# Kernel optimization log

Measured on AMD Instinct MI355X. Metric: run time of the kernel, lower is better.

The kernel has to match this reference:

```python
import jax, jax.numpy as jnp
import numpy as np

WS = 7          # window size
NH = 12         # attention heads
D_STATE = 64    # mamba d_state
HEADDIM = 64    # mamba headdim


def layernorm(x, w, b):
    mu = jnp.mean(x, axis=-1, keepdims=True)
    var = jnp.mean((x - mu) ** 2, axis=-1, keepdims=True)
    return (x - mu) * jax.lax.rsqrt(var + 1e-5) * w + b


def mamba2(x, W_in, conv_w, conv_b, dt_bias, A_log, D, mnorm_w, W_out):
    # Mamba2 (SSD) forward: in_proj -> causal depthwise conv+silu -> selective scan -> gated RMSNorm -> out_proj
    B, L, dm = x.shape
    nheads = dt_bias.shape[0]
    d_inner = nheads * HEADDIM
    zxbcdt = x @ W_in                                   # (B,L,2*d_inner+2*d_state+nheads)
    z = zxbcdt[..., :d_inner]
    xBC = zxbcdt[..., d_inner:2 * d_inner + 2 * D_STATE]
    dt = zxbcdt[..., -nheads:]
    conv_dim = xBC.shape[-1]
    pad = conv_w.shape[-1] - 1
    xBC_t = jnp.swapaxes(xBC, 1, 2)                     # (B, conv_dim, L)
    conv_out = jax.lax.conv_general_dilated(
        xBC_t, conv_w[:, None, :], window_strides=(1,), padding=[(pad, 0)],
        feature_group_count=conv_dim, dimension_numbers=('NCH', 'OIH', 'NCH'))
    xBC = jax.nn.silu(jnp.swapaxes(conv_out, 1, 2) + conv_b)
    xs = xBC[..., :d_inner]
    Bm = xBC[..., d_inner:d_inner + D_STATE]            # (B,L,n)
    Cm = xBC[..., d_inner + D_STATE:]                   # (B,L,n)
    dt = jax.nn.softplus(dt + dt_bias)                  # (B,L,h)
    A = -jnp.exp(A_log)                                 # (h,)
    dA = jnp.exp(dt * A)                                # (B,L,h)
    xh = xs.reshape(B, L, nheads, HEADDIM)              # (B,L,h,p)

    def step(h, inp):
        dA_t, dt_t, x_t, B_t, C_t = inp                 # (B,h),(B,h),(B,h,p),(B,n),(B,n)
        dBx = (dt_t[..., None] * x_t)[..., None] * B_t[:, None, None, :]
        h = h * dA_t[..., None, None] + dBx             # (B,h,p,n)
        y = jnp.einsum('bhpn,bn->bhp', h, C_t)
        return h, y

    sw = lambda a: jnp.swapaxes(a, 0, 1)                # time-major
    h0 = jnp.zeros((B, nheads, HEADDIM, D_STATE), x.dtype)
    _, ys = jax.lax.scan(step, h0, (sw(dA), sw(dt), sw(xh), sw(Bm), sw(Cm)))
    y = jnp.swapaxes(ys, 0, 1) + D[None, None, :, None] * xh   # (B,L,h,p)
    y = y.reshape(B, L, d_inner)
    g = y * jax.nn.silu(z)                              # gated RMSNorm (norm_before_gate=False)
    g = g * jax.lax.rsqrt(jnp.mean(g * g, axis=-1, keepdims=True) + 1e-5) * mnorm_w
    return g @ W_out


def gated_window_attention(xw, qkv_w, qkv_b, gate_w, gate_b, proj_w, proj_b):
    B_, N, C = xw.shape
    hd = C // NH
    qkv = (xw @ qkv_w + qkv_b).reshape(B_, N, 3, NH, hd).transpose(2, 0, 3, 1, 4)
    q, k, v = qkv[0] * (hd ** -0.5), qkv[1], qkv[2]     # (B_,h,N,d)
    attn = jax.nn.softmax(jnp.einsum('bhnd,bhmd->bhnm', q, k), axis=-1)
    xa = jnp.einsum('bhnm,bhmd->bhnd', attn, v).transpose(0, 2, 1, 3)  # (B_,N,h,d)
    gate = jax.nn.sigmoid(xw @ gate_w + gate_b)[..., None]             # (B_,N,h,1)
    xa = (xa * gate).reshape(B_, N, C)
    return xa @ proj_w + proj_b


def lgs_forward(x, norm1_w, norm1_b, W_in, conv_w, conv_b, dt_bias, A_log, D, mnorm_w, W_out,
                qkv_w, qkv_b, gate_w, gate_b, proj_w, proj_b, fusion_w, fusion_b,
                norm2_w, norm2_b, fc1_w, fc1_b, fc2_w, fc2_b, H, W):
    B, L, C = x.shape
    shortcut = x
    xn = layernorm(x, norm1_w, norm1_b)
    # Branch A: Mamba2 global scan
    x_mamba = mamba2(xn, W_in, conv_w, conv_b, dt_bias, A_log, D, mnorm_w, W_out)
    # Branch B: gated window attention (shift_size=0 -> no roll, no mask)
    x2d = xn.reshape(B, H, W, C)
    xw = x2d.reshape(B, H // WS, WS, W // WS, WS, C).transpose(0, 1, 3, 2, 4, 5).reshape(-1, WS * WS, C)
    aw = gated_window_attention(xw, qkv_w, qkv_b, gate_w, gate_b, proj_w, proj_b)
    x_attn = aw.reshape(B, H // WS, W // WS, WS, WS, C).transpose(0, 1, 3, 2, 4, 5).reshape(B, L, C)
    # Fuse branches with 1x1 conv (== linear on channel dim)
    x_cat = jnp.concatenate([x_mamba, x_attn], axis=-1)   # (B,L,2C)
    x_fused = x_cat @ fusion_w + fusion_b
    x = shortcut + x_fused
    xn2 = layernorm(x, norm2_w, norm2_b)
    mlp = jax.nn.gelu(xn2 @ fc1_w + fc1_b, approximate=False) @ fc2_w + fc2_b
    return x + mlp


def setup_inputs() -> dict:
    key = jax.random.key(0)
    ks = jax.random.split(key, 16)
    B, H, W, C = 8, 56, 56, 384
    L = H * W
    d_inner, d_state, nheads_m, d_conv = 768, 64, 12, 4
    d_in_proj = 2 * d_inner + 2 * d_state + nheads_m   # 1676
    conv_dim = d_inner + 2 * d_state                   # 896
    s = 0.02
    return {
        'x': jax.random.normal(ks[0], (B, L, C), jnp.float32),
        'norm1_w': jnp.ones((C,), jnp.float32),
        'norm1_b': jnp.zeros((C,), jnp.float32),
        'W_in': jax.random.normal(ks[1], (C, d_in_proj), jnp.float32) * s,
        'conv_w': jax.random.normal(ks[2], (conv_dim, d_conv), jnp.float32) * 0.1,
        'conv_b': jnp.zeros((conv_dim,), jnp.float32),
        'dt_bias': jax.random.normal(ks[3], (nheads_m,), jnp.float32) * 0.5,
        'A_log': jnp.log(jax.random.uniform(ks[4], (nheads_m,), jnp.float32, 1.0, 16.0)),
        'D': jnp.ones((nheads_m,), jnp.float32),
        'mnorm_w': jnp.ones((d_inner,), jnp.float32),
        'W_out': jax.random.normal(ks[5], (d_inner, C), jnp.float32) * s,
        'qkv_w': jax.random.normal(ks[6], (C, 3 * C), jnp.float32) * s,
        'qkv_b': jnp.zeros((3 * C,), jnp.float32),
        'gate_w': jax.random.normal(ks[7], (C, NH), jnp.float32) * s,
        'gate_b': jnp.zeros((NH,), jnp.float32),
        'proj_w': jax.random.normal(ks[8], (C, C), jnp.float32) * s,
        'proj_b': jnp.zeros((C,), jnp.float32),
        'fusion_w': jax.random.normal(ks[9], (2 * C, C), jnp.float32) * s,
        'fusion_b': jnp.zeros((C,), jnp.float32),
        'norm2_w': jnp.ones((C,), jnp.float32),
        'norm2_b': jnp.zeros((C,), jnp.float32),
        'fc1_w': jax.random.normal(ks[10], (C, 4 * C), jnp.float32) * s,
        'fc1_b': jnp.zeros((4 * C,), jnp.float32),
        'fc2_w': jax.random.normal(ks[11], (4 * C, C), jnp.float32) * s,
        'fc2_b': jnp.zeros((C,), jnp.float32),
        'H': H,
        'W': W,
    }


def reference(x, norm1_w, norm1_b, W_in, conv_w, conv_b, dt_bias, A_log, D, mnorm_w, W_out,
              qkv_w, qkv_b, gate_w, gate_b, proj_w, proj_b, fusion_w, fusion_b,
              norm2_w, norm2_b, fc1_w, fc1_b, fc2_w, fc2_b, H, W):
    return lgs_forward(x, norm1_w, norm1_b, W_in, conv_w, conv_b, dt_bias, A_log, D, mnorm_w, W_out,
                       qkv_w, qkv_b, gate_w, gate_b, proj_w, proj_b, fusion_w, fusion_b,
                       norm2_w, norm2_b, fc1_w, fc1_b, fc2_w, fc2_b, H, W)
```

## Files before the change

kernel.cpp:

```cpp
#include <hip/hip_runtime.h>
#include <math.h>

static constexpr int L_SEQ  = 3136;
static constexpr int NBATCH = 8;
static constexpr int CDIM   = 384;
static constexpr int DIN    = 768;
static constexpr int NHM    = 12;
static constexpr int HDM    = 64;
static constexpr int DPROJ  = 1676;
static constexpr int CONVD  = 896;
static constexpr int NROWS  = NBATCH * L_SEQ;
static constexpr int NHA    = 12;
static constexpr int NCH    = 49;
static constexpr int CHT    = 64;
static constexpr int CTK    = 28;
static constexpr int ZXLD   = 1024;

typedef __attribute__((ext_vector_type(8))) short short8;
typedef __attribute__((ext_vector_type(8))) unsigned short ushort8;
typedef __attribute__((ext_vector_type(4))) float f32x4;
typedef const unsigned int __attribute__((address_space(1)))* gua_t;
typedef unsigned int __attribute__((address_space(3)))* lua_t;

__device__ __forceinline__ float siluf(float x) { return x / (1.f + __expf(-x)); }
__device__ __forceinline__ unsigned short f2bf(float f) {
  unsigned int u = __float_as_uint(f);
  u += 0x7fff + ((u >> 16) & 1);
  return (unsigned short)(u >> 16);
}
__device__ __forceinline__ float bf2f(unsigned short h) {
  return __uint_as_float(((unsigned int)h) << 16);
}
__device__ __forceinline__ float geluf(float v) {
  float ax = fabsf(v) * 0.70710678118654752f;
  float t = __builtin_amdgcn_rcpf(fmaf(0.47047f, ax, 1.f));
  float p = t * fmaf(t, fmaf(t, 0.7478556f, -0.0958798f), 0.3480242f);
  float e = __expf(-ax * ax);
  float r = 1.f - p * e;
  float h = 0.5f * v;
  return fmaf(fabsf(h), r, h);
}
__device__ __forceinline__ unsigned int pk_bf16(float lo, float hi) {
  unsigned int d;
  asm("v_cvt_pk_bf16_f32 %0, %1, %2" : "=v"(d) : "v"(lo), "v"(hi));
  return d;
}

__global__ __launch_bounds__(256) void ln_kernel(const float* __restrict__ in,
    const float* __restrict__ w, const float* __restrict__ b, unsigned short* __restrict__ out) {
  int wave = threadIdx.x >> 6, lane = threadIdx.x & 63;
  int row = blockIdx.x * 4 + wave;
  if (row >= NROWS) return;
  const float* r = in + (size_t)row * CDIM;
  float2 v[3];
  float s1 = 0.f, s2 = 0.f;
#pragma unroll
  for (int q = 0; q < 3; q++) {
    v[q] = *(const float2*)&r[q * 128 + lane * 2];
    s1 += v[q].x + v[q].y;
    s2 += v[q].x * v[q].x + v[q].y * v[q].y;
  }
#pragma unroll
  for (int o = 32; o > 0; o >>= 1) { s1 += __shfl_xor(s1, o, 64); s2 += __shfl_xor(s2, o, 64); }
  float mu = s1 * (1.f / 384.f);
  float var = s2 * (1.f / 384.f) - mu * mu;
  float rs = rsqrtf(var + 1e-5f);
  unsigned short* o = out + (size_t)row * CDIM;
#pragma unroll
  for (int q = 0; q < 3; q++) {
    int c = q * 128 + lane * 2;
    float2 wv = *(const float2*)&w[c];
    float2 bv = *(const float2*)&b[c];
    float ox = (v[q].x - mu) * rs * wv.x + bv.x;
    float oy = (v[q].y - mu) * rs * wv.y + bv.y;
    *(unsigned int*)&o[c] = pk_bf16(ox, oy);
  }
}

__global__ __launch_bounds__(256) void wconv_kernel(const float* __restrict__ W,
    unsigned short* __restrict__ WT, int K, int N, int ldw) {
  __shared__ float tile[32][33];
  int k0 = blockIdx.x * 32, n0 = blockIdx.y * 32;
  int tx = threadIdx.x & 31, ty = threadIdx.x >> 5;
#pragma unroll
  for (int j = 0; j < 4; j++) {
    int k = k0 + ty + j * 8;
    int n = n0 + tx;
    tile[ty + j * 8][tx] = (n < N) ? W[(size_t)k * ldw + n] : 0.f;
  }
  __syncthreads();
#pragma unroll
  for (int j = 0; j < 4; j++) {
    int n = n0 + ty + j * 8;
    int k = k0 + tx;
    WT[(size_t)n * K + k] = f2bf(tile[tx][ty + j * 8]);
  }
}

template<int ACT, bool HASBIAS, bool HASRES, bool OUTBF>
__global__ __launch_bounds__(256, 4) void gemm_bf(
    const unsigned short* __restrict__ A, const unsigned short* __restrict__ WT,
    void* __restrict__ Cp, const float* __restrict__ bias,
    const float* __restrict__ res, int ldr,
    int M, int N, int K, int lda, int ldc, int coff)
{
  __shared__ unsigned short SMEM[16384];
  int t = threadIdx.x;
  int gx = gridDim.x;
  int nwg = gx * gridDim.y;
  int orig = blockIdx.y * gx + blockIdx.x;
  int qq = nwg >> 3, rr = nwg & 7;
  int xcd = orig & 7, seq = orig >> 3;
  int wgid = (xcd < rr ? xcd * (qq + 1) : rr * (qq + 1) + (xcd - rr) * qq) + seq;
  int m0 = (wgid / gx) * 128, n0 = (wgid % gx) * 128;

  int lane = t & 63, w = t >> 6;
  int wr = (w >> 1) * 64, wc = (w & 1) * 64;
  int fl = lane & 15, kq = lane >> 4;
  int so = (kq ^ ((lane >> 1) & 3)) * 8;

  int srow = t >> 2, sq = t & 3;
  int q0 = sq ^ ((srow >> 1) & 3);
  const unsigned short* pA0 = A  + (size_t)(m0 + srow) * lda + q0 * 8;
  const unsigned short* pA1 = A  + (size_t)(m0 + 64 + srow) * lda + q0 * 8;
  const unsigned short* pW0 = WT + (size_t)(n0 + srow) * K + q0 * 8;
  const unsigned short* pW1 = WT + (size_t)(n0 + 64 + srow) * K + q0 * 8;

  f32x4 acc[4][4];
#pragma unroll
  for (int i = 0; i < 4; i++)
#pragma unroll
    for (int j = 0; j < 4; j++) acc[i][j] = (f32x4)0.f;

  auto STAGE = [&](int buf) {
    unsigned short* as = SMEM + buf * 4096;
    unsigned short* ws = SMEM + 8192 + buf * 4096;
    __builtin_amdgcn_global_load_lds((gua_t)pA0, (lua_t)as + t * 4, 16, 0, 0);
    __builtin_amdgcn_global_load_lds((gua_t)pA1, (lua_t)(as + 2048) + t * 4, 16, 0, 0);
    __builtin_amdgcn_global_load_lds((gua_t)pW0, (lua_t)ws + t * 4, 16, 0, 0);
    __builtin_amdgcn_global_load_lds((gua_t)pW1, (lua_t)(ws + 2048) + t * 4, 16, 0, 0);
    pA0 += 32; pA1 += 32; pW0 += 32; pW1 += 32;
  };

  int nk = K >> 5;
  STAGE(0);
  asm volatile("s_waitcnt vmcnt(0)" ::: "memory");
  __builtin_amdgcn_s_barrier();
  asm volatile("" ::: "memory");
  __builtin_amdgcn_sched_barrier(0);
  int buf = 0;
  for (int ks = 0; ks < nk; ks++) {
    if (ks + 1 < nk) STAGE(buf ^ 1);
    const unsigned short* as = SMEM + buf * 4096;
    const unsigned short* ws = SMEM + 8192 + buf * 4096;
    short8 af[4], bfr[4];
#pragma unroll
    for (int mi = 0; mi < 4; mi++) af[mi] = *(const short8*)&as[(wr + mi * 16 + fl) * 32 + so];
#pragma unroll
    for (int ni = 0; ni < 4; ni++) bfr[ni] = *(const short8*)&ws[(wc + ni * 16 + fl) * 32 + so];
#pragma unroll
    for (int mi = 0; mi < 4; mi++)
#pragma unroll
      for (int ni = 0; ni < 4; ni++)
        acc[mi][ni] = __builtin_amdgcn_mfma_f32_16x16x32_bf16(bfr[ni], af[mi], acc[mi][ni], 0, 0, 0);
    if (ks + 1 < nk) {
      asm volatile("s_waitcnt vmcnt(0)" ::: "memory");
      __builtin_amdgcn_s_barrier();
      asm volatile("" ::: "memory");
      __builtin_amdgcn_sched_barrier(0);
      buf ^= 1;
    }
  }
  int rbase = kq * 4;
  if (OUTBF) {
    unsigned short* outp = (unsigned short*)Cp + coff;
#pragma unroll
    for (int mi = 0; mi < 4; mi++) {
      int m = m0 + wr + mi * 16 + fl;
      unsigned short* rowp = outp + (size_t)m * ldc + n0;
#pragma unroll
      for (int ni = 0; ni < 4; ni++) {
        int nb = wc + ni * 16 + rbase;
        float v0 = acc[mi][ni][0], v1 = acc[mi][ni][1];
        float v2 = acc[mi][ni][2], v3 = acc[mi][ni][3];
        if (HASBIAS) {
          float4 bv = *(const float4*)&bias[n0 + nb];
          v0 += bv.x; v1 += bv.y; v2 += bv.z; v3 += bv.w;
        }
        if (ACT == 1) { v0 = geluf(v0); v1 = geluf(v1); v2 = geluf(v2); v3 = geluf(v3); }
        uint2 pk; pk.x = pk_bf16(v0, v1); pk.y = pk_bf16(v2, v3);
        *(uint2*)&rowp[nb] = pk;
      }
    }
  } else {
    float* outp = (float*)Cp + coff;
#pragma unroll
    for (int mi = 0; mi < 4; mi++) {
      int m = m0 + wr + mi * 16 + fl;
      float* rowp = outp + (size_t)m * ldc + n0;
#pragma unroll
      for (int ni = 0; ni < 4; ni++) {
        int nb = wc + ni * 16 + rbase;
        float4 v;
        v.x = acc[mi][ni][0]; v.y = acc[mi][ni][1];
        v.z = acc[mi][ni][2]; v.w = acc[mi][ni][3];
        if (HASBIAS) {
          float4 bv = *(const float4*)&bias[n0 + nb];
          v.x += bv.x; v.y += bv.y; v.z += bv.z; v.w += bv.w;
        }
        if (ACT == 1) { v.x = geluf(v.x); v.y = geluf(v.y); v.z = geluf(v.z); v.w = geluf(v.w); }
        if (HASRES) {
          float4 rv = *(const float4*)&res[(size_t)m * ldr + n0 + nb];
          v.x += rv.x; v.y += rv.y; v.z += rv.z; v.w += rv.w;
        }
        *(float4*)&rowp[nb] = v;
      }
    }
  }
}

__global__ void dtprep_kernel(const unsigned short* __restrict__ ZX, const float* __restrict__ dt_bias,
    const float* __restrict__ A_log, float* __restrict__ DT, float* __restrict__ DA) {
  int idx = blockIdx.x * blockDim.x + threadIdx.x;
  if (idx >= NROWS * NHM) return;
  int h = idx % NHM;
  int row = idx / NHM;
  float v = bf2f(ZX[(size_t)row * ZXLD + 896 + h]) + dt_bias[h];
  float sp = (v > 20.f) ? v : log1pf(expf(v));
  DT[idx] = sp;
  DA[idx] = -expf(A_log[h]) * sp;
}

__global__ __launch_bounds__(256) void conv_bf_kernel(const unsigned short* __restrict__ xbc,
    const float* __restrict__ cw, const float* __restrict__ cb, unsigned short* __restrict__ XC,
    int ldin) {
  int t = blockIdx.x * 256 + threadIdx.x;
  int c8 = t % 112;
  int rg = t / 112;
  int b = rg / 112, lc = rg % 112;
  int l0 = lc * CTK;
  int c0 = c8 * 8;
  float w0[8], w1[8], w2[8], w3[8], bq[8];
#pragma unroll
  for (int i = 0; i < 8; i++) {
    bq[i] = cb[c0 + i];
    float4 w4 = *(const float4*)&cw[(c0 + i) * 4];
    w0[i] = w4.x; w1[i] = w4.y; w2[i] = w4.z; w3[i] = w4.w;
  }
  const unsigned short* base = xbc + (size_t)b * L_SEQ * ldin + c0;
  unsigned short* obase = XC + (size_t)b * L_SEQ * CONVD + c0;
  ushort8 h0 = (ushort8)0, h1 = (ushort8)0, h2 = (ushort8)0;
  if (l0 >= 3) {
    h0 = *(const ushort8*)&base[(size_t)(l0 - 3) * ldin];
    h1 = *(const ushort8*)&base[(size_t)(l0 - 2) * ldin];
    h2 = *(const ushort8*)&base[(size_t)(l0 - 1) * ldin];
  }
  for (int i = 0; i < CTK; i++) {
    ushort8 cur = *(const ushort8*)&base[(size_t)(l0 + i) * ldin];
    ushort8 ov;
#pragma unroll
    for (int q = 0; q < 8; q++) {
      float acc = bq[q] + w0[q] * bf2f(h0[q]) + w1[q] * bf2f(h1[q])
                + w2[q] * bf2f(h2[q]) + w3[q] * bf2f(cur[q]);
      ov[q] = f2bf(siluf(acc));
    }
    *(ushort8*)&obase[(size_t)(l0 + i) * CONVD] = ov;
    h0 = h1; h1 = h2; h2 = cur;
  }
}

__global__ __launch_bounds__(256) void mscan1_kernel(const unsigned short* __restrict__ XC,
    const float* __restrict__ dtp, const float* __restrict__ dta,
    float* __restrict__ H, float* __restrict__ QS) {
  __shared__ unsigned short Xt[64 * 72];
  __shared__ unsigned short Bt[64 * 72];
  __shared__ float lcs[64];
  __shared__ float wss[64];
  int ch = blockIdx.x, bh = blockIdx.y;
  int b = bh / NHM, head = bh - b * NHM;
  int t = threadIdx.x;
  int l0 = ch * CHT;
  const unsigned short* xcb = XC + ((size_t)b * L_SEQ + l0) * CONVD;
  if (t < 64) {
    size_t ro = ((size_t)b * L_SEQ + l0 + t) * NHM + head;
    float s = dta[ro];
#pragma unroll
    for (int o = 1; o < 64; o <<= 1) {
      float u = __shfl_up(s, o, 64);
      if (t >= o) s += u;
    }
    float lc63 = __shfl(s, 63, 64);
    lcs[t] = s;
    wss[t] = dtp[ro] * __expf(lc63 - s);
    if (t == 63) QS[bh * NCH + ch] = __expf(s);
  }
  __syncthreads();
#pragma unroll
  for (int it = 0; it < 16; it++) {
    int e = it * 256 + t;
    int j = e >> 6, cc = e & 63;
    const unsigned short* rowp = xcb + (size_t)j * CONVD;
    Xt[cc * 72 + j] = rowp[head * HDM + cc];
    Bt[cc * 72 + j] = f2bf(bf2f(rowp[768 + cc]) * wss[j]);
  }
  __syncthreads();
  int lane = t & 63, w = t >> 6;
  int wr = (w >> 1) * 32, wc = (w & 1) * 32;
  int fl = lane & 15, kq = lane >> 4;
  f32x4 acc[2][2];
#pragma unroll
  for (int i = 0; i < 2; i++)
#pragma unroll
    for (int j = 0; j < 2; j++) acc[i][j] = (f32x4)0.f;
#pragma unroll
  for (int kk = 0; kk < 2; kk++) {
    short8 af[2], bfr[2];
#pragma unroll
    for (int mi = 0; mi < 2; mi++)
      af[mi] = *(const short8*)&Xt[(wr + mi * 16 + fl) * 72 + kk * 32 + kq * 8];
#pragma unroll
    for (int ni = 0; ni < 2; ni++)
      bfr[ni] = *(const short8*)&Bt[(wc + ni * 16 + fl) * 72 + kk * 32 + kq * 8];
#pragma unroll
    for (int mi = 0; mi < 2; mi++)
#pragma unroll
      for (int ni = 0; ni < 2; ni++)
        acc[mi][ni] = __builtin_amdgcn_mfma_f32_16x16x32_bf16(af[mi], bfr[ni], acc[mi][ni], 0, 0, 0);
  }
  float* Hp = H + ((size_t)bh * NCH + ch) * 4096;
  int rbase = kq * 4, cl = fl;
#pragma unroll
  for (int mi = 0; mi < 2; mi++)
#pragma unroll
    for (int ni = 0; ni < 2; ni++)
#pragma unroll
      for (int r = 0; r < 4; r++)
        Hp[(size_t)(wr + mi * 16 + rbase + r) * 64 + wc + ni * 16 + cl] = acc[mi][ni][r];
}

__global__ __launch_bounds__(64) void scomb_kernel(float* __restrict__ H,
    const float* __restrict__ QS) {
  int bh = blockIdx.x;
  int e = (blockIdx.y * 64 + threadIdx.x) * 4;
  float4 cur = make_float4(0.f, 0.f, 0.f, 0.f);
  for (int s = 0; s < NCH; s++) {
    float* Hp = H + ((size_t)bh * NCH + s) * 4096 + e;
    float q = QS[bh * NCH + s];
    float4 tmp = *(float4*)Hp;
    *(float4*)Hp = cur;
    cur.x = q * cur.x + tmp.x;
    cur.y = q * cur.y + tmp.y;
    cur.z = q * cur.z + tmp.z;
    cur.w = q * cur.w + tmp.w;
  }
}

__global__ __launch_bounds__(256) void mscan2_kernel(const unsigned short* __restrict__ XC,
    const float* __restrict__ dtp, const float* __restrict__ dta,
    const float* __restrict__ H, const float* __restrict__ Dp,
    unsigned short* __restrict__ Ybf) {
  __shared__ unsigned short Cs[64 * 72];
  __shared__ unsigned short Bs[64 * 72];
  __shared__ unsigned short Xt[64 * 72];
  __shared__ unsigned short Hs[64 * 72];
  __shared__ unsigned short Ss[64 * 72];
  __shared__ float lcs[64];
  __shared__ float dts[64];
  int ch = blockIdx.x, bh = blockIdx.y;
  int b = bh / NHM, head = bh - b * NHM;
  int t = threadIdx.x;
  int l0 = ch * CHT;
  const unsigned short* xcb = XC + ((size_t)b * L_SEQ + l0) * CONVD;
  const float* Hg = H + ((size_t)bh * NCH + ch) * 4096;
  if (t < 64) {
    size_t ro = ((size_t)b * L_SEQ + l0 + t) * NHM + head;
    float s = dta[ro];
#pragma unroll
    for (int o = 1; o < 64; o <<= 1) {
      float u = __shfl_up(s, o, 64);
      if (t >= o) s += u;
    }
    lcs[t] = s;
    dts[t] = dtp[ro];
  }
#pragma unroll
  for (int it = 0; it < 16; it++) {
    int e = it * 256 + t;
    int j = e >> 6, cc = e & 63;
    const unsigned short* rowp = xcb + (size_t)j * CONVD;
    Xt[cc * 72 + j] = rowp[head * HDM + cc];
    Bs[j * 72 + cc] = rowp[768 + cc];
    Cs[j * 72 + cc] = rowp[832 + cc];
    Hs[j * 72 + cc] = f2bf(Hg[e]);
  }
  __syncthreads();
  int lane = t & 63, w = t >> 6;
  int wr = (w >> 1) * 32, wc = (w & 1) * 32;
  int fl = lane & 15, kq = lane >> 4;
  int rbase = kq * 4, cl = fl;
  f32x4 sacc[2][2];
#pragma unroll
  for (int i = 0; i < 2; i++)
#pragma unroll
    for (int j = 0; j < 2; j++) sacc[i][j] = (f32x4)0.f;
#pragma unroll
  for (int kk = 0; kk < 2; kk++) {
    short8 af[2], bfr[2];
#pragma unroll
    for (int mi = 0; mi < 2; mi++)
      af[mi] = *(const short8*)&Cs[(wr + mi * 16 + fl) * 72 + kk * 32 + kq * 8];
#pragma unroll
    for (int ni = 0; ni < 2; ni++)
      bfr[ni] = *(const short8*)&Bs[(wc + ni * 16 + fl) * 72 + kk * 32 + kq * 8];
#pragma unroll
    for (int mi = 0; mi < 2; mi++)
#pragma unroll
      for (int ni = 0; ni < 2; ni++)
        sacc[mi][ni] = __builtin_amdgcn_mfma_f32_16x16x32_bf16(af[mi], bfr[ni], sacc[mi][ni], 0, 0, 0);
  }
  __syncthreads();
#pragma unroll
  for (int mi = 0; mi < 2; mi++)
#pragma unroll
    for (int ni = 0; ni < 2; ni++)
#pragma unroll
      for (int r = 0; r < 4; r++) {
        int i = wr + mi * 16 + rbase + r;
        int j = wc + ni * 16 + cl;
        float v = (j <= i) ? sacc[mi][ni][r] * dts[j] * __expf(lcs[i] - lcs[j]) : 0.f;
        Ss[i * 72 + j] = f2bf(v);
      }
#pragma unroll
  for (int it = 0; it < 16; it++) {
    int e = it * 256 + t;
    int i = e >> 6, n = e & 63;
    float cv = bf2f(Cs[i * 72 + n]) * __expf(lcs[i]);
    Cs[i * 72 + n] = f2bf(cv);
  }
  __syncthreads();
  f32x4 yacc[2][2];
#pragma unroll
  for (int i = 0; i < 2; i++)
#pragma unroll
    for (int j = 0; j < 2; j++) yacc[i][j] = (f32x4)0.f;
#pragma unroll
  for (int kk = 0; kk < 2; kk++) {
    short8 af[2], bfr[2];
#pragma unroll
    for (int mi = 0; mi < 2; mi++)
      af[mi] = *(const short8*)&Ss[(wr + mi * 16 + fl) * 72 + kk * 32 + kq * 8];
#pragma unroll
    for (int ni = 0; ni < 2; ni++)
      bfr[ni] = *(const short8*)&Xt[(wc + ni * 16 + fl) * 72 + kk * 32 + kq * 8];
#pragma unroll
    for (int mi = 0; mi < 2; mi++)
#pragma unroll
      for (int ni = 0; ni < 2; ni++)
        yacc[mi][ni] = __builtin_amdgcn_mfma_f32_16x16x32_bf16(af[mi], bfr[ni], yacc[mi][ni], 0, 0, 0);
  }
#pragma unroll
  for (int kk = 0; kk < 2; kk++) {
    short8 af[2], bfr[2];
#pragma unroll
    for (int mi = 0; mi < 2; mi++)
      af[mi] = *(const short8*)&Cs[(wr + mi * 16 + fl) * 72 + kk * 32 + kq * 8];
#pragma unroll
    for (int ni = 0; ni < 2; ni++)
      bfr[ni] = *(const short8*)&Hs[(wc + ni * 16 + fl) * 72 + kk * 32 + kq * 8];
#pragma unroll
    for (int mi = 0; mi < 2; mi++)
#pragma unroll
      for (int ni = 0; ni < 2; ni++)
        yacc[mi][ni] = __builtin_amdgcn_mfma_f32_16x16x32_bf16(af[mi], bfr[ni], yacc[mi][ni], 0, 0, 0);
  }
  float Dh = Dp[head];
  unsigned short* yb = Ybf + ((size_t)b * L_SEQ + l0) * DIN + head * HDM;
#pragma unroll
  for (int mi = 0; mi < 2; mi++)
#pragma unroll
    for (int ni = 0; ni < 2; ni++)
#pragma unroll
      for (int r = 0; r < 4; r++) {
        int i = wr + mi * 16 + rbase + r;
        int p = wc + ni * 16 + cl;
        float xval = bf2f(Xt[p * 72 + i]);
        yb[(size_t)i * DIN + p] = f2bf(yacc[mi][ni][r] + Dh * xval);
      }
}

__global__ __launch_bounds__(256) void gate_rms_kernel(unsigned short* __restrict__ Y,
    const unsigned short* __restrict__ Z, const float* __restrict__ mw) {
  int wave = threadIdx.x >> 6, lane = threadIdx.x & 63;
  int row = blockIdx.x * 4 + wave;
  if (row >= NROWS) return;
  unsigned short* y = Y + (size_t)row * DIN;
  const unsigned short* z = Z + (size_t)row * DIN;
  float g[12];
  float ss = 0.f;
#pragma unroll
  for (int q = 0; q < 3; q++) {
    int c = q * 256 + lane * 4;
    uint2 yu = *(const uint2*)&y[c];
    uint2 zu = *(const uint2*)&z[c];
    float y0 = bf2f((unsigned short)(yu.x & 0xffff));
    float y1 = bf2f((unsigned short)(yu.x >> 16));
    float y2 = bf2f((unsigned short)(yu.y & 0xffff));
    float y3 = bf2f((unsigned short)(yu.y >> 16));
    float z0 = bf2f((unsigned short)(zu.x & 0xffff));
    float z1 = bf2f((unsigned short)(zu.x >> 16));
    float z2 = bf2f((unsigned short)(zu.y & 0xffff));
    float z3 = bf2f((unsigned short)(zu.y >> 16));
    float g0 = y0 * siluf(z0), g1 = y1 * siluf(z1);
    float g2 = y2 * siluf(z2), g3 = y3 * siluf(z3);
    ss += g0 * g0 + g1 * g1 + g2 * g2 + g3 * g3;
    g[q * 4 + 0] = g0; g[q * 4 + 1] = g1; g[q * 4 + 2] = g2; g[q * 4 + 3] = g3;
  }
#pragma unroll
  for (int o = 32; o > 0; o >>= 1) ss += __shfl_xor(ss, o, 64);
  float rs = rsqrtf(ss * (1.f / 768.f) + 1e-5f);
#pragma unroll
  for (int q = 0; q < 3; q++) {
    int c = q * 256 + lane * 4;
    float4 m = *(const float4*)&mw[c];
    uint2 pk;
    pk.x = pk_bf16(g[q*4+0] * rs * m.x, g[q*4+1] * rs * m.y);
    pk.y = pk_bf16(g[q*4+2] * rs * m.z, g[q*4+3] * rs * m.w);
    *(uint2*)&y[c] = pk;
  }
}

__global__ __launch_bounds__(256) void attgate_kernel(const unsigned short* __restrict__ XN,
    const float* __restrict__ gw, const float* __restrict__ gb, float* __restrict__ G) {
  int wave = threadIdx.x >> 6, lane = threadIdx.x & 63;
  int row = blockIdx.x * 4 + wave;
  if (row >= NROWS) return;
  const unsigned short* x = XN + (size_t)row * CDIM;
  float acc[12] = {};
#pragma unroll
  for (int q = 0; q < 6; q++) {
    int k = q * 64 + lane;
    float xv = bf2f(x[k]);
    const float* wr = gw + (size_t)k * 12;
    float4 w0 = *(const float4*)&wr[0];
    float4 w1 = *(const float4*)&wr[4];
    float4 w2 = *(const float4*)&wr[8];
    acc[0] += xv * w0.x; acc[1] += xv * w0.y; acc[2]  += xv * w0.z; acc[3]  += xv * w0.w;
    acc[4] += xv * w1.x; acc[5] += xv * w1.y; acc[6]  += xv * w1.z; acc[7]  += xv * w1.w;
    acc[8] += xv * w2.x; acc[9] += xv * w2.y; acc[10] += xv * w2.z; acc[11] += xv * w2.w;
  }
#pragma unroll
  for (int h = 0; h < 12; h++)
#pragma unroll
    for (int o = 32; o > 0; o >>= 1) acc[h] += __shfl_xor(acc[h], o, 64);
  if (lane == 0) {
#pragma unroll
    for (int h = 0; h < 12; h++) {
      float v = acc[h] + gb[h];
      G[(size_t)row * 12 + h] = 1.f / (1.f + expf(-v));
    }
  }
}

__global__ __launch_bounds__(64) void attn_kernel(const unsigned short* __restrict__ QKV,
    const float* __restrict__ G, unsigned short* __restrict__ XA) {
  __shared__ unsigned short Pl[64 * 72];
  __shared__ unsigned short Vt[32 * 72];
  int blk = blockIdx.x;
  int head = blk % NHA;
  int win = blk / NHA;
  int b = win >> 6;
  int wrw = win & 63;
  int wy = wrw >> 3, wx = wrw & 7;
  int lane = threadIdx.x;
  int fl = lane & 15, kq = lane >> 4;
  const float scale = 0.17677669529663688f;
  size_t bbase = (size_t)b * L_SEQ;
  const unsigned short* qb = QKV + head * 32;

  short8 aq[4], bk[4];
#pragma unroll
  for (int ti = 0; ti < 4; ti++) {
    int tok = ti * 16 + fl; if (tok > 48) tok = 48;
    int iy = tok / 7, ix = tok - iy * 7;
    size_t r = bbase + (size_t)(wy * 7 + iy) * 56 + wx * 7 + ix;
    aq[ti] = *(const short8*)&qb[r * 1152 + kq * 8];
    bk[ti] = *(const short8*)&qb[r * 1152 + 384 + kq * 8];
  }
#pragma unroll
  for (int it = 0; it < 4; it++) {
    int j = (lane >> 2) + it * 16;
    int dc = (lane & 3) * 8;
    ushort8 v8 = (ushort8)0;
    if (j <= 48) {
      int iy = j / 7, ix = j - iy * 7;
      size_t r = bbase + (size_t)(wy * 7 + iy) * 56 + wx * 7 + ix;
      v8 = *(const ushort8*)&qb[r * 1152 + 768 + dc];
    }
#pragma unroll
    for (int q2 = 0; q2 < 8; q2++) {
      int d = dc + q2;
      Vt[d * 72 + (((j >> 3) ^ (d >> 3)) << 3) + (j & 7)] = v8[q2];
    }
  }
  f32x4 sacc[4][4];
#pragma unroll
  for (int tj = 0; tj < 4; tj++)
#pragma unroll
    for (int ti = 0; ti < 4; ti++)
      sacc[tj][ti] = __builtin_amdgcn_mfma_f32_16x16x32_bf16(bk[tj], aq[ti], (f32x4)0.f, 0, 0, 0);
#pragma unroll
  for (int ti = 0; ti < 4; ti++) {
    float mx = -1e30f;
#pragma unroll
    for (int tj = 0; tj < 4; tj++)
#pragma unroll
      for (int r = 0; r < 4; r++) {
        int j = tj * 16 + kq * 4 + r;
        float v = (j < 49) ? sacc[tj][ti][r] * scale : -1e30f;
        sacc[tj][ti][r] = v;
        mx = fmaxf(mx, v);
      }
    mx = fmaxf(mx, __shfl_xor(mx, 16, 64));
    mx = fmaxf(mx, __shfl_xor(mx, 32, 64));
    float sum = 0.f;
#pragma unroll
    for (int tj = 0; tj < 4; tj++)
#pragma unroll
      for (int r = 0; r < 4; r++) {
        float e = __expf(sacc[tj][ti][r] - mx);
        sacc[tj][ti][r] = e;
        sum += e;
      }
    sum += __shfl_xor(sum, 16, 64);
    sum += __shfl_xor(sum, 32, 64);
    float inv = 1.f / sum;
    int i = ti * 16 + fl;
#pragma unroll
    for (int tj = 0; tj < 4; tj++)
#pragma unroll
      for (int r = 0; r < 4; r++) {
        int j = tj * 16 + kq * 4 + r;
        Pl[i * 72 + j] = f2bf(sacc[tj][ti][r] * inv);
      }
  }
  f32x4 oacc[4][2];
#pragma unroll
  for (int i2 = 0; i2 < 4; i2++)
#pragma unroll
    for (int nd = 0; nd < 2; nd++) oacc[i2][nd] = (f32x4)0.f;
#pragma unroll
  for (int kk = 0; kk < 2; kk++) {
    short8 ap[4], bv[2];
#pragma unroll
    for (int i2 = 0; i2 < 4; i2++)
      ap[i2] = *(const short8*)&Pl[(i2 * 16 + fl) * 72 + kk * 32 + kq * 8];
#pragma unroll
    for (int nd = 0; nd < 2; nd++) {
      int d = nd * 16 + fl;
      bv[nd] = *(const short8*)&Vt[d * 72 + (((kk * 4 + kq) ^ (d >> 3)) << 3)];
    }
#pragma unroll
    for (int i2 = 0; i2 < 4; i2++)
#pragma unroll
      for (int nd = 0; nd < 2; nd++)
        oacc[i2][nd] = __builtin_amdgcn_mfma_f32_16x16x32_bf16(ap[i2], bv[nd], oacc[i2][nd], 0, 0, 0);
  }
#pragma unroll
  for (int i2 = 0; i2 < 4; i2++) {
#pragma unroll
    for (int r = 0; r < 4; r++) {
      int i = i2 * 16 + kq * 4 + r;
      if (i > 48) continue;
      int iy = i / 7, ix = i - iy * 7;
      size_t rg = bbase + (size_t)(wy * 7 + iy) * 56 + wx * 7 + ix;
      float g = G[rg * 12 + head];
#pragma unroll
      for (int nd = 0; nd < 2; nd++)
        XA[rg * CDIM + head * 32 + nd * 16 + fl] = f2bf(oacc[i2][nd][r] * g);
    }
  }
}

extern "C" void kernel_launch(void* const* d_in, const int* in_sizes, int n_in,
                              void* d_out, int out_size, void* d_ws, size_t ws_size,
                              hipStream_t stream) {
  const float* x        = (const float*)d_in[0];
  const float* norm1_w  = (const float*)d_in[1];
  const float* norm1_b  = (const float*)d_in[2];
  const float* W_in     = (const float*)d_in[3];
  const float* conv_w   = (const float*)d_in[4];
  const float* conv_b   = (const float*)d_in[5];
  const float* dt_bias  = (const float*)d_in[6];
  const float* A_log    = (const float*)d_in[7];
  const float* Dp       = (const float*)d_in[8];
  const float* mnorm_w  = (const float*)d_in[9];
  const float* W_out    = (const float*)d_in[10];
  const float* qkv_w    = (const float*)d_in[11];
  const float* qkv_b    = (const float*)d_in[12];
  const float* gate_w   = (const float*)d_in[13];
  const float* gate_b   = (const float*)d_in[14];
  const float* proj_w   = (const float*)d_in[15];
  const float* proj_b   = (const float*)d_in[16];
  const float* fusion_w = (const float*)d_in[17];
  const float* fusion_b = (const float*)d_in[18];
  const float* norm2_w  = (const float*)d_in[19];
  const float* norm2_b  = (const float*)d_in[20];
  const float* fc1_w    = (const float*)d_in[21];
  const float* fc1_b    = (const float*)d_in[22];
  const float* fc2_w    = (const float*)d_in[23];
  const float* fc2_b    = (const float*)d_in[24];
  float* OUT = (float*)d_out;

  float* ws = (float*)d_ws;
  unsigned short* XNBF = (unsigned short*)ws;
  float* XC_  = ws + 4816896;
  float* SCR  = XC_ + 22478848;
  unsigned short* YBF = (unsigned short*)(SCR + 22478848);
  unsigned short* WT  = (unsigned short*)(SCR + 22478848 + 9633792);
  float* DT_ = (float*)(WT + 3047424);
  float* DA_ = DT_ + 301056;
  float* G_  = DA_ + 301056;
  float* QS_ = G_  + 301056;

  unsigned short* ZXBF  = (unsigned short*)SCR;
  unsigned short* XCBF  = (unsigned short*)XC_;
  float* H_ = SCR;
  unsigned short* ZBF   = (unsigned short*)SCR;
  unsigned short* QKVBF = (unsigned short*)SCR;
  unsigned short* M1BF  = (unsigned short*)SCR;
  unsigned short* CATBF = (unsigned short*)XC_;
  unsigned short* XABF  = (unsigned short*)(XC_ + 9633792);

  unsigned short* wt_xbcdt = WT;
  unsigned short* wt_z    = WT + 393216;
  unsigned short* wt_out  = WT + 688128;
  unsigned short* wt_qkv  = WT + 983040;
  unsigned short* wt_proj = WT + 1425408;
  unsigned short* wt_fus  = WT + 1572864;
  unsigned short* wt_fc1  = WT + 1867776;
  unsigned short* wt_fc2  = WT + 2457600;

  wconv_kernel<<<dim3(12,  29), 256, 0, stream>>>(W_in + 768,  wt_xbcdt, 384, 908, DPROJ);
  wconv_kernel<<<dim3(12,  24), 256, 0, stream>>>(W_in,        wt_z,    384,  768, DPROJ);
  wconv_kernel<<<dim3(24,  12), 256, 0, stream>>>(W_out,       wt_out,  768,  384, 384);
  wconv_kernel<<<dim3(12,  36), 256, 0, stream>>>(qkv_w,       wt_qkv,  384, 1152, 1152);
  wconv_kernel<<<dim3(12,  12), 256, 0, stream>>>(proj_w,      wt_proj, 384,  384, 384);
  wconv_kernel<<<dim3(24,  12), 256, 0, stream>>>(fusion_w,    wt_fus,  768,  384, 384);
  wconv_kernel<<<dim3(12,  48), 256, 0, stream>>>(fc1_w,       wt_fc1,  384, 1536, 1536);
  wconv_kernel<<<dim3(48,  12), 256, 0, stream>>>(fc2_w,       wt_fc2, 1536,  384, 384);

  ln_kernel<<<6272, 256, 0, stream>>>(x, norm1_w, norm1_b, XNBF);

  gemm_bf<0, false, false, true><<<dim3(8, 196), 256, 0, stream>>>(
      XNBF, wt_xbcdt, ZXBF, nullptr, nullptr, 0, NROWS, 908, CDIM, CDIM, ZXLD, 0);
  conv_bf_kernel<<<392, 256, 0, stream>>>(ZXBF, conv_w, conv_b, XCBF, ZXLD);
  dtprep_kernel<<<(NROWS * NHM + 255) / 256, 256, 0, stream>>>(ZXBF, dt_bias, A_log, DT_, DA_);

  mscan1_kernel<<<dim3(NCH, 96), 256, 0, stream>>>(XCBF, DT_, DA_, H_, QS_);
  scomb_kernel<<<dim3(96, 16), 64, 0, stream>>>(H_, QS_);
  mscan2_kernel<<<dim3(NCH, 96), 256, 0, stream>>>(XCBF, DT_, DA_, H_, Dp, YBF);

  gemm_bf<0, false, false, true><<<dim3(6, 196), 256, 0, stream>>>(
      XNBF, wt_z, ZBF, nullptr, nullptr, 0, NROWS, DIN, CDIM, CDIM, DIN, 0);
  gate_rms_kernel<<<6272, 256, 0, stream>>>(YBF, ZBF, mnorm_w);

  gemm_bf<0, false, false, true><<<dim3(3, 196), 256, 0, stream>>>(
      YBF, wt_out, CATBF, nullptr, nullptr, 0, NROWS, CDIM, DIN, DIN, 2 * CDIM, 0);

  attgate_kernel<<<6272, 256, 0, stream>>>(XNBF, gate_w, gate_b, G_);

  gemm_bf<0, true, false, true><<<dim3(9, 196), 256, 0, stream>>>(
      XNBF, wt_qkv, QKVBF, qkv_b, nullptr, 0, NROWS, 3 * CDIM, CDIM, CDIM, 3 * CDIM, 0);
  attn_kernel<<<512 * NHA, 64, 0, stream>>>(QKVBF, G_, XABF);

  gemm_bf<0, true, false, true><<<dim3(3, 196), 256, 0, stream>>>(
      XABF, wt_proj, CATBF, proj_b, nullptr, 0, NROWS, CDIM, CDIM, CDIM, 2 * CDIM, CDIM);

  gemm_bf<0, true, true, false><<<dim3(3, 196), 256, 0, stream>>>(
      CATBF, wt_fus, OUT, fusion_b, x, CDIM, NROWS, CDIM, 2 * CDIM, 2 * CDIM, CDIM, 0);

  ln_kernel<<<6272, 256, 0, stream>>>(OUT, norm2_w, norm2_b, XNBF);

  gemm_bf<1, true, false, true><<<dim3(12, 196), 256, 0, stream>>>(
      XNBF, wt_fc1, M1BF, fc1_b, nullptr, 0, NROWS, 4 * CDIM, CDIM, CDIM, 4 * CDIM, 0);
  gemm_bf<0, true, true, false><<<dim3(3, 196), 256, 0, stream>>>(
      M1BF, wt_fc2, OUT, fc2_b, OUT, CDIM, NROWS, CDIM, 4 * CDIM, 4 * CDIM, CDIM, 0);
}
```

Measured before the change: 664.7 us.

## Triple-buffer GEMM K-loop and stage bf16 epilogue through LDS for coalesced stores

The bf16 GEMM moves from double to triple buffering in shared memory, with two stages in flight and a partial vmcnt wait, so global loads overlap compute across more iterations and the loop uses one barrier per step. The bf16-output epilogue now writes results into swizzled LDS, then stores full contiguous row segments to global memory instead of scattered 8-byte stores. LDS use rises from 32KB to 48KB per block, which may reduce occupancy under launch_bounds(256,4). The epilogue also adds two syncthreads.

Result: no change. 656.2 us (-1.3%).

```diff
diff --git a/kernel.cpp b/kernel.cpp
--- a/kernel.cpp
+++ b/kernel.cpp
@@ -104,7 +104,7 @@
     const float* __restrict__ res, int ldr,
     int M, int N, int K, int lda, int ldc, int coff)
 {
-  __shared__ unsigned short SMEM[16384];
+  __shared__ unsigned short SMEM[24576];
   int t = threadIdx.x;
   int gx = gridDim.x;
   int nwg = gx * gridDim.y;
@@ -134,7 +134,7 @@
 
   auto STAGE = [&](int buf) {
     unsigned short* as = SMEM + buf * 4096;
-    unsigned short* ws = SMEM + 8192 + buf * 4096;
+    unsigned short* ws = SMEM + 12288 + buf * 4096;
     __builtin_amdgcn_global_load_lds((gua_t)pA0, (lua_t)as + t * 4, 16, 0, 0);
     __builtin_amdgcn_global_load_lds((gua_t)pA1, (lua_t)(as + 2048) + t * 4, 16, 0, 0);
     __builtin_amdgcn_global_load_lds((gua_t)pW0, (lua_t)ws + t * 4, 16, 0, 0);
@@ -144,15 +144,24 @@
 
   int nk = K >> 5;
   STAGE(0);
-  asm volatile("s_waitcnt vmcnt(0)" ::: "memory");
-  __builtin_amdgcn_s_barrier();
-  asm volatile("" ::: "memory");
-  __builtin_amdgcn_sched_barrier(0);
-  int buf = 0;
+  STAGE(1);
+  int cb = 0, sb = 2;
   for (int ks = 0; ks < nk; ks++) {
-    if (ks + 1 < nk) STAGE(buf ^ 1);
-    const unsigned short* as = SMEM + buf * 4096;
-    const unsigned short* ws = SMEM + 8192 + buf * 4096;
+    if (ks + 1 < nk) {
+      asm volatile("s_waitcnt vmcnt(4)" ::: "memory");
+    } else {
+      asm volatile("s_waitcnt vmcnt(0)" ::: "memory");
+    }
+    __builtin_amdgcn_s_barrier();
+    asm volatile("" ::: "memory");
+    __builtin_amdgcn_sched_barrier(0);
+    if (ks + 2 < nk) {
+      STAGE(sb);
+      sb = sb == 2 ? 0 : sb + 1;
+    }
+    const unsigned short* as = SMEM + cb * 4096;
+    const unsigned short* ws = SMEM + 12288 + cb * 4096;
+    cb = cb == 2 ? 0 : cb + 1;
     short8 af[4], bfr[4];
 #pragma unroll
     for (int mi = 0; mi < 4; mi++) af[mi] = *(const short8*)&as[(wr + mi * 16 + fl) * 32 + so];
@@ -163,36 +172,40 @@
 #pragma unroll
       for (int ni = 0; ni < 4; ni++)
         acc[mi][ni] = __builtin_amdgcn_mfma_f32_16x16x32_bf16(bfr[ni], af[mi], acc[mi][ni], 0, 0, 0);
-    if (ks + 1 < nk) {
-      asm volatile("s_waitcnt vmcnt(0)" ::: "memory");
-      __builtin_amdgcn_s_barrier();
-      asm volatile("" ::: "memory");
-      __builtin_amdgcn_sched_barrier(0);
-      buf ^= 1;
-    }
-  }
-  int rbase = kq * 4;
+  }
   if (OUTBF) {
-    unsigned short* outp = (unsigned short*)Cp + coff;
+    __syncthreads();
+    float4 bv[4];
+    if (HASBIAS) {
+#pragma unroll
+      for (int ni = 0; ni < 4; ni++) bv[ni] = *(const float4*)&bias[n0 + wc + ni * 16 + kq * 4];
+    }
 #pragma unroll
     for (int mi = 0; mi < 4; mi++) {
-      int m = m0 + wr + mi * 16 + fl;
-      unsigned short* rowp = outp + (size_t)m * ldc + n0;
+      int mloc = wr + mi * 16 + fl;
 #pragma unroll
       for (int ni = 0; ni < 4; ni++) {
-        int nb = wc + ni * 16 + rbase;
         float v0 = acc[mi][ni][0], v1 = acc[mi][ni][1];
         float v2 = acc[mi][ni][2], v3 = acc[mi][ni][3];
-        if (HASBIAS) {
-          float4 bv = *(const float4*)&bias[n0 + nb];
-          v0 += bv.x; v1 += bv.y; v2 += bv.z; v3 += bv.w;
-        }
+        if (HASBIAS) { v0 += bv[ni].x; v1 += bv[ni].y; v2 += bv[ni].z; v3 += bv[ni].w; }
         if (ACT == 1) { v0 = geluf(v0); v1 = geluf(v1); v2 = geluf(v2); v3 = geluf(v3); }
+        int gidx = (wc >> 2) + ni * 4 + kq;
+        int gs = gidx ^ (mloc & 15);
         uint2 pk; pk.x = pk_bf16(v0, v1); pk.y = pk_bf16(v2, v3);
-        *(uint2*)&rowp[nb] = pk;
+        *(uint2*)&SMEM[mloc * 128 + gs * 4] = pk;
       }
     }
+    __syncthreads();
+    unsigned short* outp = (unsigned short*)Cp + coff + n0;
+#pragma unroll
+    for (int it2 = 0; it2 < 16; it2++) {
+      int gg = it2 * 256 + t;
+      int row = gg >> 5, g = gg & 31;
+      uint2 v = *(const uint2*)&SMEM[row * 128 + (g ^ (row & 15)) * 4];
+      *(uint2*)&outp[(size_t)(m0 + row) * ldc + g * 4] = v;
+    }
   } else {
+    int rbase = kq * 4;
     float* outp = (float*)Cp + coff;
 #pragma unroll
     for (int mi = 0; mi < 4; mi++) {
@@ -205,8 +218,8 @@
         v.x = acc[mi][ni][0]; v.y = acc[mi][ni][1];
         v.z = acc[mi][ni][2]; v.w = acc[mi][ni][3];
         if (HASBIAS) {
-          float4 bv = *(const float4*)&bias[n0 + nb];
-          v.x += bv.x; v.y += bv.y; v.z += bv.z; v.w += bv.w;
+          float4 bvv = *(const float4*)&bias[n0 + nb];
+          v.x += bvv.x; v.y += bvv.y; v.z += bvv.z; v.w += bvv.w;
         }
         if (ACT == 1) { v.x = geluf(v.x); v.y = geluf(v.y); v.z = geluf(v.z); v.w = geluf(v.w); }
         if (HASRES) {
```
